# Performance work log

Hardware: AMD Instinct MI355X
Metric: run time of the kernel (lower is better)

## Reference

```python
import jax, jax.numpy as jnp
import numpy as np

N_NODES = 100000
D_FEAT = 128
K_NEIGH = 16
N_LAYERS = 2
F_OUT = 128  # features = [128, 128]


def setup_inputs() -> dict:
    key = jax.random.key(0)
    k1, k2, k3 = jax.random.split(key, 3)
    feats = jax.random.normal(k1, (N_NODES, D_FEAT), dtype=jnp.float32)
    # per-layer sampled neighbor indices (fresh sampling each layer, as in the source)
    neigh_idx = jax.random.randint(k2, (N_LAYERS, N_NODES, K_NEIGH), 0, N_NODES, dtype=jnp.int32)
    # Dense kernels: input is concat(self, mean_neighbors) -> 2*D; both layers 256 -> 128
    Ws = jax.random.normal(k3, (N_LAYERS, 2 * D_FEAT, F_OUT), dtype=jnp.float32) * (1.0 / np.sqrt(2 * D_FEAT))
    bs = jnp.zeros((N_LAYERS, F_OUT), dtype=jnp.float32)
    return {"feats": feats, "neigh_idx": neigh_idx, "Ws": Ws, "bs": bs}


def reference(feats, neigh_idx, Ws, bs):
    """GraphSAGE (mean aggregator): per layer, gather sampled neighbors,
    mean-aggregate, concat with self, Dense; relu between layers.
    Returns the last-layer Dense output (pre-relu), matching `new_feats`
    returned by the source module.
    """
    h = feats  # [N, D]
    z = h
    for l in range(Ws.shape[0]):
        neigh = h[neigh_idx[l]]              # [N, K, D] irregular gather
        agg = neigh.mean(axis=1)             # [N, D] mean aggregation
        cat = jnp.concatenate([h, agg], axis=-1)  # [N, 2D]
        z = cat @ Ws[l] + bs[l]              # [N, F]
        h = jax.nn.relu(z)
    return z
```

## Files before the change

### kernel.cpp

```cpp
#include <hip/hip_runtime.h>

#define N_NODES 100000
#define D 128
#define K 16
#define CATK 256
#define MB 32
#define PAD 8
#define LDSW (CATK + PAD)
#define ZW 132

typedef __attribute__((ext_vector_type(8))) short bf16x8;
typedef __attribute__((ext_vector_type(4))) float f32x4;
typedef __attribute__((ext_vector_type(2))) float f32x2;

__device__ __forceinline__ unsigned short f2bf(float f) {
    union { float f; unsigned u; } v; v.f = f;
    unsigned u = v.u;
    return (unsigned short)((u + 0x7fffu + ((u >> 16) & 1u)) >> 16);
}

__device__ __forceinline__ unsigned pk4(float a, float b, float c, float d) {
    int w = __builtin_amdgcn_cvt_pk_fp8_f32(a, b, 0, false);
    w = __builtin_amdgcn_cvt_pk_fp8_f32(c, d, w, true);
    return (unsigned)w;
}

__device__ __forceinline__ void dec4p(unsigned w, f32x2* a) {
    f32x2 lo = __builtin_amdgcn_cvt_pk_f32_fp8((int)w, false);
    f32x2 hi = __builtin_amdgcn_cvt_pk_f32_fp8((int)w, true);
    a[0] += lo;
    a[1] += hi;
}

__global__ void cvt_all(const float* __restrict__ feats, const float* __restrict__ Ws,
                        unsigned* __restrict__ f8, unsigned short* __restrict__ Wt) {
    int tid = blockIdx.x * 256 + threadIdx.x;
    int i = tid * 16;
    if (i < N_NODES * D) {
        const float4* p = (const float4*)(feats + i);
        float4 v0 = p[0], v1 = p[1], v2 = p[2], v3 = p[3];
        uint4 o;
        o.x = pk4(v0.x, v0.y, v0.z, v0.w);
        o.y = pk4(v1.x, v1.y, v1.z, v1.w);
        o.z = pk4(v2.x, v2.y, v2.z, v2.w);
        o.w = pk4(v3.x, v3.y, v3.z, v3.w);
        *(uint4*)(f8 + i / 4) = o;
    }
    if (tid < 2 * CATK * D) {
        int l = tid / (CATK * D);
        int r = tid % (CATK * D);
        int n = r / CATK, k = r % CATK;
        Wt[tid] = f2bf(Ws[l * CATK * D + k * D + n]);
    }
}

__launch_bounds__(256, 4)
__global__ void gather_mean(const unsigned char* __restrict__ g8,
                            const int* __restrict__ idx,
                            unsigned short* __restrict__ agg) {
    const int t = threadIdx.x;
    const int m = t >> 3;
    const int c = (t & 7) * 16;
    const int node = blockIdx.x * MB + m;

    const int4* ip = (const int4*)(idx + (size_t)node * K);
    int4 i0 = ip[0], i1 = ip[1];

    const unsigned char* gp = g8 + c;
    f32x2 acc2[8];
#pragma unroll
    for (int j = 0; j < 8; ++j) acc2[j] = (f32x2){0.f, 0.f};

    {
        uint4 u[8];
        u[0] = *(const uint4*)(gp + (size_t)i0.x * D);
        u[1] = *(const uint4*)(gp + (size_t)i0.y * D);
        u[2] = *(const uint4*)(gp + (size_t)i0.z * D);
        u[3] = *(const uint4*)(gp + (size_t)i0.w * D);
        u[4] = *(const uint4*)(gp + (size_t)i1.x * D);
        u[5] = *(const uint4*)(gp + (size_t)i1.y * D);
        u[6] = *(const uint4*)(gp + (size_t)i1.z * D);
        u[7] = *(const uint4*)(gp + (size_t)i1.w * D);
        int4 i2 = ip[2], i3 = ip[3];
#pragma unroll
        for (int k = 0; k < 8; ++k) {
            dec4p(u[k].x, acc2 + 0);
            dec4p(u[k].y, acc2 + 2);
            dec4p(u[k].z, acc2 + 4);
            dec4p(u[k].w, acc2 + 6);
        }
        u[0] = *(const uint4*)(gp + (size_t)i2.x * D);
        u[1] = *(const uint4*)(gp + (size_t)i2.y * D);
        u[2] = *(const uint4*)(gp + (size_t)i2.z * D);
        u[3] = *(const uint4*)(gp + (size_t)i2.w * D);
        u[4] = *(const uint4*)(gp + (size_t)i3.x * D);
        u[5] = *(const uint4*)(gp + (size_t)i3.y * D);
        u[6] = *(const uint4*)(gp + (size_t)i3.z * D);
        u[7] = *(const uint4*)(gp + (size_t)i3.w * D);
#pragma unroll
        for (int k = 0; k < 8; ++k) {
            dec4p(u[k].x, acc2 + 0);
            dec4p(u[k].y, acc2 + 2);
            dec4p(u[k].z, acc2 + 4);
            dec4p(u[k].w, acc2 + 6);
        }
    }

    unsigned pk[8];
#pragma unroll
    for (int j = 0; j < 8; ++j) {
        unsigned short a = f2bf(acc2[j].x * (1.f / 16.f));
        unsigned short b = f2bf(acc2[j].y * (1.f / 16.f));
        pk[j] = (unsigned)a | ((unsigned)b << 16);
    }
    unsigned short* op = agg + (size_t)node * D + c;
    *(uint4*)op       = make_uint4(pk[0], pk[1], pk[2], pk[3]);
    *(uint4*)(op + 8) = make_uint4(pk[4], pk[5], pk[6], pk[7]);
}

template <int LAYER>
__launch_bounds__(256, 4)
__global__ void sage_mm(const float* __restrict__ self_f32,
                        const unsigned short* __restrict__ self_bf,
                        const unsigned short* __restrict__ agg,
                        const unsigned short* __restrict__ Wt,
                        const float* __restrict__ bias,
                        unsigned short* __restrict__ h_out,
                        unsigned char* __restrict__ h8_out,
                        float* __restrict__ z_out) {
    __shared__ __align__(16) char smraw[MB * LDSW * 2];
    unsigned short (*cat)[LDSW] = (unsigned short (*)[LDSW])smraw;
    float (*zb)[ZW] = (float (*)[ZW])smraw;

    const int t = threadIdx.x;
    const int base = blockIdx.x * MB;
    const int lane = t & 63;
    const int wave = t >> 6;
    const int q = lane >> 4;
    const int nlo = lane & 15;

    {
        const int m = t >> 3;
        const int c = (t & 7) * 16;
        const int node = base + m;

        const uint4* ap = (const uint4*)(agg + (size_t)node * D + c);
        uint4 a0 = ap[0], a1 = ap[1];

        if (LAYER == 0) {
            const float4* sp = (const float4*)(self_f32 + (size_t)node * D + c);
            float sv[16];
            *(f32x4*)&sv[0]  = *(const f32x4*)&sp[0];
            *(f32x4*)&sv[4]  = *(const f32x4*)&sp[1];
            *(f32x4*)&sv[8]  = *(const f32x4*)&sp[2];
            *(f32x4*)&sv[12] = *(const f32x4*)&sp[3];
            unsigned w[8];
#pragma unroll
            for (int j = 0; j < 8; ++j)
                w[j] = (unsigned)f2bf(sv[2 * j]) | ((unsigned)f2bf(sv[2 * j + 1]) << 16);
            *(uint4*)&cat[m][c]     = make_uint4(w[0], w[1], w[2], w[3]);
            *(uint4*)&cat[m][c + 8] = make_uint4(w[4], w[5], w[6], w[7]);
        } else {
            const uint4* sp = (const uint4*)(self_bf + (size_t)node * D + c);
            uint4 sb0 = sp[0], sb1 = sp[1];
            *(uint4*)&cat[m][c]     = sb0;
            *(uint4*)&cat[m][c + 8] = sb1;
        }

        *(uint4*)&cat[m][D + c]     = a0;
        *(uint4*)&cat[m][D + c + 8] = a1;
    }

    bf16x8 bfrag[2][8];
#pragma unroll
    for (int ct = 0; ct < 2; ++ct) {
        int n = wave * 32 + ct * 16 + nlo;
        const unsigned short* wp = Wt + n * CATK + q * 8;
#pragma unroll
        for (int ks = 0; ks < 8; ++ks)
            bfrag[ct][ks] = *(const bf16x8*)(wp + ks * 32);
    }

    __syncthreads();

    f32x4 acc00 = {}, acc01 = {}, acc10 = {}, acc11 = {};
#pragma unroll
    for (int ks = 0; ks < 8; ++ks) {
        bf16x8 a0 = *(const bf16x8*)&cat[nlo][ks * 32 + q * 8];
        bf16x8 a1 = *(const bf16x8*)&cat[16 + nlo][ks * 32 + q * 8];
        acc00 = __builtin_amdgcn_mfma_f32_16x16x32_bf16(a0, bfrag[0][ks], acc00, 0, 0, 0);
        acc01 = __builtin_amdgcn_mfma_f32_16x16x32_bf16(a0, bfrag[1][ks], acc01, 0, 0, 0);
        acc10 = __builtin_amdgcn_mfma_f32_16x16x32_bf16(a1, bfrag[0][ks], acc10, 0, 0, 0);
        acc11 = __builtin_amdgcn_mfma_f32_16x16x32_bf16(a1, bfrag[1][ks], acc11, 0, 0, 0);
    }

    if (LAYER == 1) {
#pragma unroll
        for (int ct = 0; ct < 2; ++ct) {
            int col = wave * 32 + ct * 16 + nlo;
            float bv = bias[col];
            f32x4 v0 = (ct == 0) ? acc00 : acc01;
            f32x4 v1 = (ct == 0) ? acc10 : acc11;
#pragma unroll
            for (int r = 0; r < 4; ++r) {
                z_out[(size_t)(base + q * 4 + r) * D + col]      = v0[r] + bv;
                z_out[(size_t)(base + 16 + q * 4 + r) * D + col] = v1[r] + bv;
            }
        }
        return;
    }

    __syncthreads();
#pragma unroll
    for (int ct = 0; ct < 2; ++ct) {
        int col = wave * 32 + ct * 16 + nlo;
        float bv = bias[col];
        f32x4 v0 = (ct == 0) ? acc00 : acc01;
        f32x4 v1 = (ct == 0) ? acc10 : acc11;
#pragma unroll
        for (int r = 0; r < 4; ++r) {
            zb[q * 4 + r][col]      = v0[r] + bv;
            zb[16 + q * 4 + r][col] = v1[r] + bv;
        }
    }
    __syncthreads();
    {
        const int m = t >> 3;
        const int c = (t & 7) * 16;
        float x[16];
        *(f32x4*)&x[0]  = *(const f32x4*)&zb[m][c];
        *(f32x4*)&x[4]  = *(const f32x4*)&zb[m][c + 4];
        *(f32x4*)&x[8]  = *(const f32x4*)&zb[m][c + 8];
        *(f32x4*)&x[12] = *(const f32x4*)&zb[m][c + 12];
        size_t go = (size_t)(base + m) * D + c;
#pragma unroll
        for (int i = 0; i < 16; ++i) x[i] = x[i] > 0.f ? x[i] : 0.f;
        unsigned wb[8];
#pragma unroll
        for (int j = 0; j < 8; ++j)
            wb[j] = (unsigned)f2bf(x[2 * j]) | ((unsigned)f2bf(x[2 * j + 1]) << 16);
        uint4* hp = (uint4*)(h_out + go);
        hp[0] = make_uint4(wb[0], wb[1], wb[2], wb[3]);
        hp[1] = make_uint4(wb[4], wb[5], wb[6], wb[7]);
        uint4 o8;
        o8.x = pk4(x[0], x[1], x[2], x[3]);
        o8.y = pk4(x[4], x[5], x[6], x[7]);
        o8.z = pk4(x[8], x[9], x[10], x[11]);
        o8.w = pk4(x[12], x[13], x[14], x[15]);
        *(uint4*)(h8_out + go) = o8;
    }
}

extern "C" void kernel_launch(void* const* d_in, const int* in_sizes, int n_in,
                              void* d_out, int out_size, void* d_ws, size_t ws_size,
                              hipStream_t stream) {
    const float* feats = (const float*)d_in[0];
    const int* neigh   = (const int*)d_in[1];
    const float* Ws    = (const float*)d_in[2];
    const float* bs    = (const float*)d_in[3];
    float* out = (float*)d_out;

    char* ws = (char*)d_ws;
    unsigned short* h1_bf  = (unsigned short*)(ws);
    unsigned char*  feats8 = (unsigned char*)(ws + 25600000);
    unsigned char*  h18    = (unsigned char*)(ws + 38400000);
    unsigned short* Wt     = (unsigned short*)(ws + 51200000);
    unsigned short* agg    = (unsigned short*)(ws + 51331072);

    cvt_all<<<3125, 256, 0, stream>>>(feats, Ws, (unsigned*)feats8, Wt);

    gather_mean<<<N_NODES / MB, 256, 0, stream>>>(feats8, neigh, agg);
    sage_mm<0><<<N_NODES / MB, 256, 0, stream>>>(
        feats, nullptr, agg, Wt, bs, h1_bf, h18, nullptr);

    gather_mean<<<N_NODES / MB, 256, 0, stream>>>(h18, neigh + N_NODES * K, agg);
    sage_mm<1><<<N_NODES / MB, 256, 0, stream>>>(
        nullptr, h1_bf, agg, Wt + CATK * D, bs + D,
        nullptr, nullptr, out);
}
```

Before: 219.7 us.

## Partition fp8 feature table into column groups mapped to XCD pairs for gather locality

The fp8 feature tables and the aggregate buffer are stored as four column groups of 32 bytes per node instead of one 128-byte row. The gather kernel assigns each column group to a pair of XCDs (by workgroup index modulo 8), so each XCD's L2 only needs to cache a quarter of the table. Each thread now handles half of a group for one node, with 128 nodes per block. The producer kernels write in the grouped layout. The change relies on round-robin workgroup-to-XCD dispatch and leaves each random access a 32-byte sector, which risks worse DRAM efficiency.

Result: slower. 239.2 us (+8.9%).

```diff
diff --git a/kernel.cpp b/kernel.cpp
--- a/kernel.cpp
+++ b/kernel.cpp
@@ -8,6 +8,8 @@
 #define PAD 8
 #define LDSW (CATK + PAD)
 #define ZW 132
+#define GW 32
+#define NGRP 4
 
 typedef __attribute__((ext_vector_type(8))) short bf16x8;
 typedef __attribute__((ext_vector_type(4))) float f32x4;
@@ -33,7 +35,7 @@
 }
 
 __global__ void cvt_all(const float* __restrict__ feats, const float* __restrict__ Ws,
-                        unsigned* __restrict__ f8, unsigned short* __restrict__ Wt) {
+                        unsigned char* __restrict__ f8c, unsigned short* __restrict__ Wt) {
     int tid = blockIdx.x * 256 + threadIdx.x;
     int i = tid * 16;
     if (i < N_NODES * D) {
@@ -44,7 +46,8 @@
         o.y = pk4(v1.x, v1.y, v1.z, v1.w);
         o.z = pk4(v2.x, v2.y, v2.z, v2.w);
         o.w = pk4(v3.x, v3.y, v3.z, v3.w);
-        *(uint4*)(f8 + i / 4) = o;
+        int node = tid >> 3, sub = tid & 7;
+        *(uint4*)(f8c + ((size_t)(sub >> 1) * N_NODES + node) * GW + (sub & 1) * 16) = o;
     }
     if (tid < 2 * CATK * D) {
         int l = tid / (CATK * D);
@@ -55,32 +58,37 @@
 }
 
 __launch_bounds__(256, 4)
-__global__ void gather_mean(const unsigned char* __restrict__ g8,
+__global__ void gather_mean(const unsigned char* __restrict__ g8c,
                             const int* __restrict__ idx,
-                            unsigned short* __restrict__ agg) {
+                            unsigned short* __restrict__ aggc) {
     const int t = threadIdx.x;
-    const int m = t >> 3;
-    const int c = (t & 7) * 16;
-    const int node = blockIdx.x * MB + m;
+    const int wg = blockIdx.x;
+    const int xcd = wg & 7;
+    const int grp = xcd >> 1;
+    const int nodeblk = (wg >> 3) * 2 + (xcd & 1);
+    const int m = t >> 1;
+    const int h = t & 1;
+    const int node = nodeblk * 128 + m;
+    if (node >= N_NODES) return;
 
     const int4* ip = (const int4*)(idx + (size_t)node * K);
     int4 i0 = ip[0], i1 = ip[1];
 
-    const unsigned char* gp = g8 + c;
+    const unsigned char* gp = g8c + (size_t)grp * N_NODES * GW + h * 16;
     f32x2 acc2[8];
 #pragma unroll
     for (int j = 0; j < 8; ++j) acc2[j] = (f32x2){0.f, 0.f};
 
     {
         uint4 u[8];
-        u[0] = *(const uint4*)(gp + (size_t)i0.x * D);
-        u[1] = *(const uint4*)(gp + (size_t)i0.y * D);
-        u[2] = *(const uint4*)(gp + (size_t)i0.z * D);
-        u[3] = *(const uint4*)(gp + (size_t)i0.w * D);
-        u[4] = *(const uint4*)(gp + (size_t)i1.x * D);
-        u[5] = *(const uint4*)(gp + (size_t)i1.y * D);
-        u[6] = *(const uint4*)(gp + (size_t)i1.z * D);
-        u[7] = *(const uint4*)(gp + (size_t)i1.w * D);
+        u[0] = *(const uint4*)(gp + (size_t)i0.x * GW);
+        u[1] = *(const uint4*)(gp + (size_t)i0.y * GW);
+        u[2] = *(const uint4*)(gp + (size_t)i0.z * GW);
+        u[3] = *(const uint4*)(gp + (size_t)i0.w * GW);
+        u[4] = *(const uint4*)(gp + (size_t)i1.x * GW);
+        u[5] = *(const uint4*)(gp + (size_t)i1.y * GW);
+        u[6] = *(const uint4*)(gp + (size_t)i1.z * GW);
+        u[7] = *(const uint4*)(gp + (size_t)i1.w * GW);
         int4 i2 = ip[2], i3 = ip[3];
 #pragma unroll
         for (int k = 0; k < 8; ++k) {
@@ -89,14 +97,14 @@
             dec4p(u[k].z, acc2 + 4);
             dec4p(u[k].w, acc2 + 6);
         }
-        u[0] = *(const uint4*)(gp + (size_t)i2.x * D);
-        u[1] = *(const uint4*)(gp + (size_t)i2.y * D);
-        u[2] = *(const uint4*)(gp + (size_t)i2.z * D);
-        u[3] = *(const uint4*)(gp + (size_t)i2.w * D);
-        u[4] = *(const uint4*)(gp + (size_t)i3.x * D);
-        u[5] = *(const uint4*)(gp + (size_t)i3.y * D);
-        u[6] = *(const uint4*)(gp + (size_t)i3.z * D);
-        u[7] = *(const uint4*)(gp + (size_t)i3.w * D);
+        u[0] = *(const uint4*)(gp + (size_t)i2.x * GW);
+        u[1] = *(const uint4*)(gp + (size_t)i2.y * GW);
+        u[2] = *(const uint4*)(gp + (size_t)i2.z * GW);
+        u[3] = *(const uint4*)(gp + (size_t)i2.w * GW);
+        u[4] = *(const uint4*)(gp + (size_t)i3.x * GW);
+        u[5] = *(const uint4*)(gp + (size_t)i3.y * GW);
+        u[6] = *(const uint4*)(gp + (size_t)i3.z * GW);
+        u[7] = *(const uint4*)(gp + (size_t)i3.w * GW);
 #pragma unroll
         for (int k = 0; k < 8; ++k) {
             dec4p(u[k].x, acc2 + 0);
@@ -113,7 +121,7 @@
         unsigned short b = f2bf(acc2[j].y * (1.f / 16.f));
         pk[j] = (unsigned)a | ((unsigned)b << 16);
     }
-    unsigned short* op = agg + (size_t)node * D + c;
+    unsigned short* op = aggc + ((size_t)grp * N_NODES + node) * GW + h * 16;
     *(uint4*)op       = make_uint4(pk[0], pk[1], pk[2], pk[3]);
     *(uint4*)(op + 8) = make_uint4(pk[4], pk[5], pk[6], pk[7]);
 }
@@ -122,11 +130,11 @@
 __launch_bounds__(256, 4)
 __global__ void sage_mm(const float* __restrict__ self_f32,
                         const unsigned short* __restrict__ self_bf,
-                        const unsigned short* __restrict__ agg,
+                        const unsigned short* __restrict__ aggc,
                         const unsigned short* __restrict__ Wt,
                         const float* __restrict__ bias,
                         unsigned short* __restrict__ h_out,
-                        unsigned char* __restrict__ h8_out,
+                        unsigned char* __restrict__ h8c_out,
                         float* __restrict__ z_out) {
     __shared__ __align__(16) char smraw[MB * LDSW * 2];
     unsigned short (*cat)[LDSW] = (unsigned short (*)[LDSW])smraw;
@@ -143,8 +151,9 @@
         const int m = t >> 3;
         const int c = (t & 7) * 16;
         const int node = base + m;
-
-        const uint4* ap = (const uint4*)(agg + (size_t)node * D + c);
+        const int sub = t & 7;
+
+        const uint4* ap = (const uint4*)(aggc + ((size_t)(sub >> 1) * N_NODES + node) * GW + (sub & 1) * 16);
         uint4 a0 = ap[0], a1 = ap[1];
 
         if (LAYER == 0) {
@@ -227,6 +236,7 @@
     {
         const int m = t >> 3;
         const int c = (t & 7) * 16;
+        const int sub = t & 7;
         float x[16];
         *(f32x4*)&x[0]  = *(const f32x4*)&zb[m][c];
         *(f32x4*)&x[4]  = *(const f32x4*)&zb[m][c + 4];
@@ -247,7 +257,7 @@
         o8.y = pk4(x[4], x[5], x[6], x[7]);
         o8.z = pk4(x[8], x[9], x[10], x[11]);
         o8.w = pk4(x[12], x[13], x[14], x[15]);
-        *(uint4*)(h8_out + go) = o8;
+        *(uint4*)(h8c_out + ((size_t)(sub >> 1) * N_NODES + (size_t)(base + m)) * GW + (sub & 1) * 16) = o8;
     }
 }
 
@@ -267,13 +277,13 @@
     unsigned short* Wt     = (unsigned short*)(ws + 51200000);
     unsigned short* agg    = (unsigned short*)(ws + 51331072);
 
-    cvt_all<<<3125, 256, 0, stream>>>(feats, Ws, (unsigned*)feats8, Wt);
-
-    gather_mean<<<N_NODES / MB, 256, 0, stream>>>(feats8, neigh, agg);
+    cvt_all<<<3125, 256, 0, stream>>>(feats, Ws, feats8, Wt);
+
+    gather_mean<<<3128, 256, 0, stream>>>(feats8, neigh, agg);
     sage_mm<0><<<N_NODES / MB, 256, 0, stream>>>(
         feats, nullptr, agg, Wt, bs, h1_bf, h18, nullptr);
 
-    gather_mean<<<N_NODES / MB, 256, 0, stream>>>(h18, neigh + N_NODES * K, agg);
+    gather_mean<<<3128, 256, 0, stream>>>(h18, neigh + N_NODES * K, agg);
     sage_mm<1><<<N_NODES / MB, 256, 0, stream>>>(
         nullptr, h1_bf, agg, Wt + CATK * D, bs + D,
         nullptr, nullptr, out);
```
